# Performance work log

Measured on AMD Instinct MI355X. Metric: run time of the kernel, lower is better.

Reference implementation:

```python
import jax, jax.numpy as jnp
import numpy as np
from jax import lax

B, N, C = 8, 3136, 512
NUM_HEADS = 8
HEAD_DIM = C // NUM_HEADS
KS = 5  # depthwise conv kernel size


def setup_inputs() -> dict:
    key = jax.random.key(0)
    ks = jax.random.split(key, 8)
    s = 0.02
    return {
        "x": jax.random.normal(ks[0], (B, N, C), dtype=jnp.float32),
        "H": 56,
        "W": 56,
        "Wq": jax.random.normal(ks[1], (C, C), dtype=jnp.float32) * s,
        "Wkv": jax.random.normal(ks[2], (C, 2 * C), dtype=jnp.float32) * s,
        "pos_enc": jnp.zeros((1, N, C), dtype=jnp.float32),
        "dwc_w": jax.random.normal(ks[3], (HEAD_DIM, 1, KS, KS), dtype=jnp.float32) * s,
        "dwc_b": jnp.zeros((HEAD_DIM,), dtype=jnp.float32),
        "Wproj": jax.random.normal(ks[4], (C, C), dtype=jnp.float32) * s,
        "bproj": jnp.zeros((C,), dtype=jnp.float32),
    }


def _split_heads(t):
    # (B, N, C) -> (B*h, N, head_dim), matching 'b n (h c) -> (b h) n c'
    b, n, c = t.shape
    return t.reshape(b, n, NUM_HEADS, HEAD_DIM).transpose(0, 2, 1, 3).reshape(b * NUM_HEADS, n, HEAD_DIM)


def reference(x, H, W, Wq, Wkv, pos_enc, dwc_w, dwc_b, Wproj, bproj):
    b, n, c = x.shape
    # projections (qkv_bias=False)
    q = jnp.maximum(x @ Wq, 0.0)                       # ReLU kernel feature map
    kv = x @ Wkv
    k = jnp.maximum(kv[..., :c] + pos_enc, 0.0)
    v = kv[..., c:]

    q = _split_heads(q)  # (bh, n, d)
    k = _split_heads(k)
    v = _split_heads(v)

    # normalizer z_i = 1 / (q_i . sum_j k_j + eps)
    z = 1.0 / (jnp.einsum('bic,bc->bi', q, k.sum(axis=1)) + 1e-6)
    # kv-first ordering (i*j*(c+d) > c*d*(i+j) for these shapes)
    kvmat = jnp.einsum('bjc,bjd->bcd', k, v)           # (bh, d, d)
    out = jnp.einsum('bic,bcd->bid', q, kvmat) * z[..., None]

    # depthwise conv residual on v: 'b (w h) c -> b c w h'
    num = int(round(n ** 0.5))
    fmap = v.reshape(-1, num, num, HEAD_DIM).transpose(0, 3, 1, 2)  # (bh, d, num, num)
    fmap = lax.conv_general_dilated(
        fmap, dwc_w, window_strides=(1, 1), padding='SAME',
        feature_group_count=HEAD_DIM,
        dimension_numbers=('NCHW', 'OIHW', 'NCHW'))
    fmap = fmap + dwc_b[None, :, None, None]
    fmap = fmap.transpose(0, 2, 3, 1).reshape(-1, n, HEAD_DIM)
    out = out + fmap

    # merge heads: '(b h) n c -> b n (h c)'
    out = out.reshape(b, NUM_HEADS, n, HEAD_DIM).transpose(0, 2, 1, 3).reshape(b, n, c)
    return out @ Wproj + bproj
```

## Files before the change

### kernel.cpp

```cpp
#include <hip/hip_runtime.h>
#include <stdint.h>

#define B_    8
#define N_    3136
#define C_    512
#define MTOT  25088

typedef __attribute__((ext_vector_type(8))) short bf16x8;
typedef __attribute__((ext_vector_type(4))) float f32x4;

__device__ __forceinline__ float bf2f(short s){
  union { float f; uint32_t u; } cv; cv.u = ((uint32_t)(uint16_t)s) << 16; return cv.f;
}
__device__ __forceinline__ short f2bf(float f){
  union { float f; uint32_t u; } cv; cv.f = f;
  uint32_t r = cv.u + 0x7FFFu + ((cv.u >> 16) & 1u);
  return (short)(r >> 16);
}

typedef const __attribute__((address_space(1))) void* gas1_t;
typedef __attribute__((address_space(3))) void* las3_t;
__device__ __forceinline__ void gld16(const void* g, void* l){
  __builtin_amdgcn_global_load_lds((gas1_t)g, (las3_t)l, 16, 0, 0);
}

#define BARR  __builtin_amdgcn_s_barrier()
#define SCHB  __builtin_amdgcn_sched_barrier(0)
#define VMC0  asm volatile("s_waitcnt vmcnt(0)" ::: "memory")
#define VMC4  asm volatile("s_waitcnt vmcnt(4)" ::: "memory")
#define VMC6  asm volatile("s_waitcnt vmcnt(6)" ::: "memory")
#define LGKM0  asm volatile("s_waitcnt lgkmcnt(0)" ::: "memory")
#define LGKM2  asm volatile("s_waitcnt lgkmcnt(2)" ::: "memory")
#define LGKM10 asm volatile("s_waitcnt lgkmcnt(10)" ::: "memory")

__global__ __launch_bounds__(256) void cvt_x(const float* __restrict__ x,
                                             short* __restrict__ xb, int n8){
  int i = blockIdx.x * 256 + threadIdx.x;
  if (i >= n8) return;
  const float4* p = (const float4*)x;
  float4 a = p[i*2], b = p[i*2+1];
  short o[8] = { f2bf(a.x), f2bf(a.y), f2bf(a.z), f2bf(a.w),
                 f2bf(b.x), f2bf(b.y), f2bf(b.z), f2bf(b.w) };
  *(bf16x8*)(xb + i*8) = *(bf16x8*)o;
}

__global__ __launch_bounds__(256) void tconv(const float* __restrict__ src,
                                             short* __restrict__ dst, int J){
  __shared__ float tile[32][33];
  int jb = blockIdx.x * 32, kb = blockIdx.y * 32;
  int tx = threadIdx.x & 31, ty = threadIdx.x >> 5;
#pragma unroll
  for (int r = 0; r < 32; r += 8)
    tile[ty + r][tx] = src[(size_t)(kb + ty + r) * J + jb + tx];
  __syncthreads();
#pragma unroll
  for (int r = 0; r < 32; r += 8)
    dst[(size_t)(jb + ty + r) * 512 + kb + tx] = f2bf(tile[tx][ty + r]);
}

__global__ __launch_bounds__(256) void conv_wT(const float* __restrict__ w,
                                               float* __restrict__ wt){
  int i = blockIdx.x * 256 + threadIdx.x;
  if (i < 1600) { int c = i / 25, tap = i - c * 25; wt[tap * 64 + c] = w[i]; }
}

template<int MODE, int NCT>
__global__ __launch_bounds__(512, 2)
void gemm_bf16(const short* __restrict__ A, const short* __restrict__ Bt,
               short* __restrict__ oQ, short* __restrict__ oK, short* __restrict__ oV,
               const float* __restrict__ posenc,
               float* __restrict__ oF, const float* __restrict__ bias)
{
  extern __shared__ __align__(16) char lds[];
  const int tid = threadIdx.x;
  const int wave = tid >> 6, lane = tid & 63;
  const int fr = lane & 15;

  constexpr int nwg = 98 * NCT;
  constexpr int q8 = nwg / 8, r8 = nwg % 8;
  const int orig = blockIdx.x;
  const int xcd = orig & 7, lid = orig >> 3;
  const int swz = (xcd < r8 ? xcd * (q8 + 1) : r8 * (q8 + 1) + (xcd - r8) * q8) + lid;
  const int rt = (swz / NCT) * 256;
  const int ct = (swz % NCT) * 256;

  const int wm = (wave >> 2) * 128;
  const int wn = (wave & 3) * 64;

  const int srow = lane >> 2;
  const int csrc = ((lane & 3) ^ ((lane >> 3) & 3)) << 3;
  const short* srcA = A  + (size_t)(rt + wave * 32 + srow) * 512 + csrc;
  const short* srcB = Bt + (size_t)(ct + wave * 32 + srow) * 512 + csrc;
  char* dA = lds + wave * 2048;
  char* dB = lds + 32768 + wave * 2048;

  auto stage = [&](int sbb, int isB, int ks, int tt) {
    const short* s = (isB ? srcB : srcA) + tt * 64 + ks * 32;
    char* d = (isB ? dB : dA) + sbb + ks * 16384;
    gld16(s,        d);
    gld16(s + 8192, d + 1024);
  };

  const int cR   = (((lane >> 4) ^ ((fr >> 1) & 3)) << 4);
  const int offA = (wm + fr) * 64 + cR;
  const int offB = 32768 + (wn + fr) * 64 + cR;

#define READ_A(dst, bufb, ks) do { \
    const char* _p = lds + (bufb) + (ks) * 16384 + offA; \
    _Pragma("unroll") \
    for (int _i = 0; _i < 8; _i++) dst[_i] = *(const bf16x8*)(_p + _i * 1024); \
  } while (0)
#define READ_B2(dst, bufb, ks, j0) do { \
    const char* _p = lds + (bufb) + (ks) * 16384 + offB + (j0) * 1024; \
    dst[0] = *(const bf16x8*)(_p); \
    dst[1] = *(const bf16x8*)(_p + 1024); \
  } while (0)
#define MFMA16(afv, bv, jb) do { \
    __builtin_amdgcn_s_setprio(1); \
    _Pragma("unroll") \
    for (int _i = 0; _i < 8; _i++) { \
      acc[_i][jb]     = __builtin_amdgcn_mfma_f32_16x16x32_bf16(afv[_i], bv[0], acc[_i][jb],     0, 0, 0); \
      acc[_i][jb + 1] = __builtin_amdgcn_mfma_f32_16x16x32_bf16(afv[_i], bv[1], acc[_i][jb + 1], 0, 0, 0); \
    } \
    __builtin_amdgcn_s_setprio(0); \
  } while (0)

  f32x4 zv = {0.f, 0.f, 0.f, 0.f};
  f32x4 acc[8][4];
#pragma unroll
  for (int i = 0; i < 8; i++)
#pragma unroll
    for (int j = 0; j < 4; j++) acc[i][j] = zv;

  bf16x8 afU[8], afV[8], bX[2], bY[2];

  stage(0, 0, 0, 0); stage(0, 1, 0, 0); stage(0, 0, 1, 0); stage(0, 1, 1, 0);
  VMC4; BARR; SCHB;
  READ_A(afU, 0, 0);
  READ_B2(bX, 0, 0, 0);

  for (int t = 0; t < 7; ++t) {
    const int bufb = (t & 1) * 65536, sbb = bufb ^ 65536;
    stage(sbb, 0, 0, t + 1);
    VMC6; BARR; SCHB;
    READ_B2(bY, bufb, 0, 2);
    LGKM2; SCHB;
    MFMA16(afU, bX, 0);
    stage(sbb, 1, 0, t + 1);
    VMC4; BARR; SCHB;
    READ_A(afV, bufb, 1);
    READ_B2(bX, bufb, 1, 0);
    LGKM10; SCHB;
    MFMA16(afU, bY, 2);
    stage(sbb, 0, 1, t + 1);
    VMC6; BARR; SCHB;
    READ_B2(bY, bufb, 1, 2);
    LGKM2; SCHB;
    MFMA16(afV, bX, 0);
    stage(sbb, 1, 1, t + 1);
    VMC4; BARR; SCHB;
    READ_A(afU, sbb, 0);
    READ_B2(bX, sbb, 0, 0);
    LGKM10; SCHB;
    MFMA16(afV, bY, 2);
  }
  {
    const int bufb = 65536;
    VMC4; BARR; SCHB;
    READ_B2(bY, bufb, 0, 2);
    LGKM2; SCHB;
    MFMA16(afU, bX, 0);
    VMC0; BARR; SCHB;
    READ_A(afV, bufb, 1);
    READ_B2(bX, bufb, 1, 0);
    LGKM10; SCHB;
    MFMA16(afU, bY, 2);
    READ_B2(bY, bufb, 1, 2);
    LGKM2; SCHB;
    MFMA16(afV, bX, 0);
    LGKM0; SCHB;
    MFMA16(afV, bY, 2);
  }

  BARR; SCHB;

  const int rb = (lane >> 4) << 2;
  if (MODE == 0) {
    short* ov = (short*)lds;
    const int sel = ct >> 9;
    const int cb  = ct - sel * 512;
    short* outp = sel == 0 ? oQ : (sel == 1 ? oK : oV);
#pragma unroll
    for (int q4 = 0; q4 < 4; ++q4) {
      if (q4) __syncthreads();
      if ((wave >> 2) == (q4 >> 1)) {
        const int ib = (q4 & 1) * 4;
#pragma unroll
        for (int ii = 0; ii < 4; ii++)
#pragma unroll
          for (int j = 0; j < 4; j++)
#pragma unroll
            for (int r = 0; r < 4; r++)
              ov[(ii * 16 + rb + r) * 260 + wn + j * 16 + fr] = f2bf(acc[ib + ii][j][r]);
      }
      __syncthreads();
#pragma unroll
      for (int p = 0; p < 4; ++p) {
        int id = tid + 512 * p;
        int row = id >> 5, cc = (id & 31) * 8;
        bf16x8 vv = *(const bf16x8*)&ov[row * 260 + cc];
        int grow = rt + q4 * 64 + row;
        short o[8];
        if (sel == 0) {
#pragma unroll
          for (int e = 0; e < 8; e++) o[e] = f2bf(fmaxf(bf2f(vv[e]), 0.f));
        } else if (sel == 1) {
          int nr = grow % N_;
          const float* pp = posenc + (size_t)nr * 512 + cb + cc;
          f32x4 p0 = *(const f32x4*)pp;
          f32x4 p1 = *(const f32x4*)(pp + 4);
#pragma unroll
          for (int e = 0; e < 4; e++) {
            o[e]     = f2bf(fmaxf(bf2f(vv[e]) + p0[e], 0.f));
            o[e + 4] = f2bf(fmaxf(bf2f(vv[e + 4]) + p1[e], 0.f));
          }
        } else {
#pragma unroll
          for (int e = 0; e < 8; e++) o[e] = vv[e];
        }
        *(bf16x8*)(outp + (size_t)grow * 512 + cb + cc) = *(bf16x8*)o;
      }
    }
  } else {
    float* ovf = (float*)lds;
#pragma unroll
    for (int q4 = 0; q4 < 4; ++q4) {
      if (q4) __syncthreads();
      if ((wave >> 2) == (q4 >> 1)) {
        const int ib = (q4 & 1) * 4;
#pragma unroll
        for (int ii = 0; ii < 4; ii++)
#pragma unroll
          for (int j = 0; j < 4; j++)
#pragma unroll
            for (int r = 0; r < 4; r++)
              ovf[(ii * 16 + rb + r) * 260 + wn + j * 16 + fr] = acc[ib + ii][j][r];
      }
      __syncthreads();
#pragma unroll
      for (int p = 0; p < 4; ++p) {
        int id = tid + 512 * p;
        int row = id >> 5, cc = (id & 31) * 8;
        f32x4 v0 = *(const f32x4*)&ovf[row * 260 + cc];
        f32x4 v1 = *(const f32x4*)&ovf[row * 260 + cc + 4];
        v0 += *(const f32x4*)&bias[ct + cc];
        v1 += *(const f32x4*)&bias[ct + cc + 4];
        float* op = oF + (size_t)(rt + q4 * 64 + row) * 512 + ct + cc;
        *(f32x4*)op       = v0;
        *(f32x4*)(op + 4) = v1;
      }
    }
  }
#undef READ_A
#undef READ_B2
#undef MFMA16
}

__global__ __launch_bounds__(256)
void kvmat_part(const short* __restrict__ kb, const short* __restrict__ vb,
                float* __restrict__ pKV, float* __restrict__ pKS)
{
  __shared__ __align__(16) float lk[64][64];
  __shared__ __align__(16) float lv[64][64];
  const int chunk = blockIdx.x, bh = blockIdx.y;
  const int b = bh >> 3, h = bh & 7;
  const int t = threadIdx.x;
  const int tc = t >> 4, td = t & 15;
  const int kc = t & 63, kr = (t >> 6) * 16;
  float acc[4][4] = {};
  float ksacc = 0.f;

  for (int tile = 0; tile < 7; ++tile) {
    const int r0 = chunk * 448 + tile * 64;
    __syncthreads();
#pragma unroll
    for (int i = 0; i < 2; i++) {
      int idx = t + i * 256;
      int r = idx >> 3, c8 = (idx & 7) << 3;
      size_t g = (size_t)(b * N_ + r0 + r) * 512 + h * 64 + c8;
      bf16x8 kk = *(const bf16x8*)(kb + g);
      bf16x8 vv = *(const bf16x8*)(vb + g);
#pragma unroll
      for (int e = 0; e < 8; e++) { lk[r][c8 + e] = bf2f(kk[e]); lv[r][c8 + e] = bf2f(vv[e]); }
    }
    __syncthreads();
#pragma unroll 4
    for (int r = 0; r < 64; r++) {
      f32x4 k4 = *(const f32x4*)&lk[r][tc * 4];
      f32x4 v4 = *(const f32x4*)&lv[r][td * 4];
#pragma unroll
      for (int i = 0; i < 4; i++)
#pragma unroll
        for (int j = 0; j < 4; j++) acc[i][j] += k4[i] * v4[j];
    }
#pragma unroll 4
    for (int rr = 0; rr < 16; rr++) ksacc += lk[kr + rr][kc];
  }

  const int pbase = (bh * 7 + chunk) * 4096;
#pragma unroll
  for (int i = 0; i < 4; i++)
#pragma unroll
    for (int j = 0; j < 4; j++)
      pKV[pbase + (tc * 4 + i) * 64 + td * 4 + j] = acc[i][j];
  __syncthreads();
  float* red = &lk[0][0];
  red[t] = ksacc;
  __syncthreads();
  if (t < 64)
    pKS[(bh * 7 + chunk) * 64 + t] = red[t] + red[t + 64] + red[t + 128] + red[t + 192];
}

__global__ __launch_bounds__(256)
void kv_reduce(const float* __restrict__ pKV, const float* __restrict__ pKS,
               float* __restrict__ kvm, float* __restrict__ ksum)
{
  int bh = blockIdx.x, t = threadIdx.x;
#pragma unroll
  for (int i = 0; i < 16; i++) {
    int idx = t + i * 256;
    float s = 0.f;
#pragma unroll
    for (int c = 0; c < 7; c++) s += pKV[(bh * 7 + c) * 4096 + idx];
    kvm[bh * 4096 + idx] = s;
  }
  if (t < 64) {
    float s = 0.f;
#pragma unroll
    for (int c = 0; c < 7; c++) s += pKS[(bh * 7 + c) * 64 + t];
    ksum[bh * 64 + t] = s;
  }
}

__global__ __launch_bounds__(256)
void conv_dw(const short* __restrict__ vb, const float* __restrict__ wT,
             const float* __restrict__ bias, short* __restrict__ pre)
{
  __shared__ __align__(16) short lsv[5 * 56 * 64];
  __shared__ __align__(16) float lwT[25 * 64];
  const int y = blockIdx.x, bh = blockIdx.y;
  const int b = bh >> 3, h = bh & 7;
  const int t = threadIdx.x;
  for (int i = t; i < 1600; i += 256) lwT[i] = wT[i];
  for (int i = t; i < 2240; i += 256) {
    int row = i / 448, rem = i - row * 448;
    int xx = rem >> 3, c8i = rem & 7;
    int gy = y + row - 2;
    bf16x8 val = {0, 0, 0, 0, 0, 0, 0, 0};
    if ((unsigned)gy < 56u)
      val = *(const bf16x8*)(vb + (size_t)(b * N_ + gy * 56 + xx) * 512 + h * 64 + c8i * 8);
    *(bf16x8*)(lsv + i * 8) = val;
  }
  __syncthreads();

  const int c8 = t & 7;
  const int x0 = t >> 3;
  float acc0[8], acc1[8];
  {
    f32x4 b0 = *(const f32x4*)&bias[c8 * 8];
    f32x4 b1 = *(const f32x4*)&bias[c8 * 8 + 4];
#pragma unroll
    for (int e = 0; e < 4; e++) { acc0[e] = b0[e]; acc0[e+4] = b1[e];
                                  acc1[e] = b0[e]; acc1[e+4] = b1[e]; }
  }
#pragma unroll
  for (int dy = 0; dy < 5; ++dy) {
#pragma unroll
    for (int dx = 0; dx < 5; ++dx) {
      float w8[8];
      {
        const float* wp = &lwT[(dy * 5 + dx) * 64 + c8 * 8];
        *(f32x4*)&w8[0] = *(const f32x4*)wp;
        *(f32x4*)&w8[4] = *(const f32x4*)(wp + 4);
      }
      const int base = dy * 56 * 64 + c8 * 8;
      int xxa = x0 + dx - 2;
      if ((unsigned)xxa < 56u) {
        bf16x8 v = *(const bf16x8*)(lsv + base + xxa * 64);
#pragma unroll
        for (int e = 0; e < 8; e++) acc0[e] += bf2f(v[e]) * w8[e];
      }
      int xxb = xxa + 32;
      if (xxb < 56) {
        bf16x8 v = *(const bf16x8*)(lsv + base + xxb * 64);
#pragma unroll
        for (int e = 0; e < 8; e++) acc1[e] += bf2f(v[e]) * w8[e];
      }
    }
  }
  size_t gbase = (size_t)(b * N_ + y * 56 + x0) * 512 + h * 64 + c8 * 8;
  short o[8];
#pragma unroll
  for (int e = 0; e < 8; e++) o[e] = f2bf(acc0[e]);
  *(bf16x8*)(pre + gbase) = *(bf16x8*)o;
  if (x0 + 32 < 56) {
#pragma unroll
    for (int e = 0; e < 8; e++) o[e] = f2bf(acc1[e]);
    *(bf16x8*)(pre + gbase + (size_t)32 * 512) = *(bf16x8*)o;
  }
}

__global__ __launch_bounds__(256)
void attn_comb(const short* __restrict__ qb, const float* __restrict__ kvm,
               const float* __restrict__ ksum, short* __restrict__ pre)
{
  __shared__ __align__(16) float lkv[4096];
  __shared__ __align__(16) float lq[4096];
  __shared__ float lks[64];
  const int pt = blockIdx.x, bh = blockIdx.y;
  const int b = bh >> 3, h = bh & 7;
  const int t = threadIdx.x;
  for (int i = t; i < 4096; i += 256) lkv[i] = kvm[bh * 4096 + i];
  if (t < 64) lks[t] = ksum[bh * 64 + t];
  {
    const int p = t & 63, cg = t >> 6;
    size_t g = (size_t)(b * N_ + pt * 64 + p) * 512 + h * 64 + cg * 16;
    bf16x8 qa = *(const bf16x8*)(qb + g);
    bf16x8 qc = *(const bf16x8*)(qb + g + 8);
#pragma unroll
    for (int e = 0; e < 8; e++) {
      lq[(cg * 16 + e) * 64 + p]     = bf2f(qa[e]);
      lq[(cg * 16 + 8 + e) * 64 + p] = bf2f(qc[e]);
    }
  }
  __syncthreads();
  const int p = t & 63, d0 = (t >> 6) * 16;
  float acc[16] = {};
  float zd = 0.f;
#pragma unroll 4
  for (int c = 0; c < 64; c++) {
    float qv = lq[c * 64 + p];
    zd += qv * lks[c];
    const f32x4* row = (const f32x4*)&lkv[c * 64 + d0];
    f32x4 m0 = row[0], m1 = row[1], m2 = row[2], m3 = row[3];
#pragma unroll
    for (int e = 0; e < 4; e++) {
      acc[e]      += qv * m0[e];
      acc[4 + e]  += qv * m1[e];
      acc[8 + e]  += qv * m2[e];
      acc[12 + e] += qv * m3[e];
    }
  }
  float z = 1.f / (zd + 1e-6f);
  size_t base = (size_t)(b * N_ + pt * 64 + p) * 512 + h * 64 + d0;
  bf16x8 f0 = *(const bf16x8*)(pre + base);
  bf16x8 f1 = *(const bf16x8*)(pre + base + 8);
  short o[16];
#pragma unroll
  for (int e = 0; e < 8; e++) {
    o[e]     = f2bf(acc[e] * z + bf2f(f0[e]));
    o[e + 8] = f2bf(acc[e + 8] * z + bf2f(f1[e]));
  }
  *(bf16x8*)(pre + base)     = *(bf16x8*)&o[0];
  *(bf16x8*)(pre + base + 8) = *(bf16x8*)&o[8];
}

extern "C" void kernel_launch(void* const* d_in, const int* in_sizes, int n_in,
                              void* d_out, int out_size, void* d_ws, size_t ws_size,
                              hipStream_t stream)
{
  const float* x     = (const float*)d_in[0];
  const float* Wq    = (const float*)d_in[3];
  const float* Wkv   = (const float*)d_in[4];
  const float* pos   = (const float*)d_in[5];
  const float* dwcw  = (const float*)d_in[6];
  const float* dwcb  = (const float*)d_in[7];
  const float* Wproj = (const float*)d_in[8];
  const float* bproj = (const float*)d_in[9];
  float* out = (float*)d_out;

  char* ws = (char*)d_ws;
  size_t off = 0;
  auto alloc = [&](size_t bytes) -> void* {
    void* p = ws + off;
    off = (off + bytes + 255) & ~(size_t)255;
    return p;
  };
  short* xb     = (short*)alloc((size_t)MTOT * 512 * 2);
  short* wqkvT  = (short*)alloc((size_t)1536 * 512 * 2);
  short* wprojT = (short*)alloc((size_t)512 * 512 * 2);
  float* wTc    = (float*)alloc((size_t)25 * 64 * 4);
  short* qb     = (short*)alloc((size_t)MTOT * 512 * 2);
  short* kbuf   = (short*)alloc((size_t)MTOT * 512 * 2);
  short* vbuf   = (short*)alloc((size_t)MTOT * 512 * 2);
  float* pKV    = (float*)alloc((size_t)64 * 7 * 4096 * 4);
  float* pKS    = (float*)alloc((size_t)64 * 7 * 64 * 4);
  float* kvm    = (float*)alloc((size_t)64 * 4096 * 4);
  float* ksumB  = (float*)alloc((size_t)64 * 64 * 4);
  short* pre    = (short*)alloc((size_t)MTOT * 512 * 2);
  if (ws_size < off) return;

  {
    auto k0 = gemm_bf16<0, 6>;
    auto k1 = gemm_bf16<1, 2>;
    hipFuncSetAttribute(reinterpret_cast<const void*>(k0),
                        hipFuncAttributeMaxDynamicSharedMemorySize, 131072);
    hipFuncSetAttribute(reinterpret_cast<const void*>(k1),
                        hipFuncAttributeMaxDynamicSharedMemorySize, 131072);
  }

  cvt_x<<<dim3((MTOT * 512 / 8 + 255) / 256), dim3(256), 0, stream>>>(x, xb, MTOT * 512 / 8);
  conv_wT<<<dim3(7), dim3(256), 0, stream>>>(dwcw, wTc);
  tconv<<<dim3(16, 16), dim3(256), 0, stream>>>(Wq,    wqkvT,              512);
  tconv<<<dim3(32, 16), dim3(256), 0, stream>>>(Wkv,   wqkvT + 512 * 512, 1024);
  tconv<<<dim3(16, 16), dim3(256), 0, stream>>>(Wproj, wprojT,             512);
  gemm_bf16<0, 6><<<dim3(588), dim3(512), 131072, stream>>>(xb, wqkvT, qb, kbuf, vbuf, pos,
                                                            nullptr, nullptr);
  kvmat_part<<<dim3(7, 64), dim3(256), 0, stream>>>(kbuf, vbuf, pKV, pKS);
  kv_reduce<<<dim3(64), dim3(256), 0, stream>>>(pKV, pKS, kvm, ksumB);
  conv_dw<<<dim3(56, 64), dim3(256), 0, stream>>>(vbuf, wTc, dwcb, pre);
  attn_comb<<<dim3(49, 64), dim3(256), 0, stream>>>(qb, kvm, ksumB, pre);
  gemm_bf16<1, 2><<<dim3(196), dim3(512), 131072, stream>>>(pre, wprojT, nullptr, nullptr, nullptr,
                                                            nullptr, out, bproj);
}
```

Baseline: 234.1 us.

## Compute q·kvmat with bf16 MFMA using a transposed bf16 kv matrix

kv_reduce now writes the per-head kv matrix as a transposed bf16 array instead of fp32. The attention-combine kernel is replaced by a single-wavefront MFMA kernel that loads q and kvT fragments directly from global memory. It then stages the results through LDS for coalesced residual add and store. This removes the scalar FMA loop and the fp32 LDS staging of q and kv, at the cost of rounding kvmat to bf16 and using small 64-thread blocks.

```diff
diff --git a/kernel.cpp b/kernel.cpp
--- a/kernel.cpp
+++ b/kernel.cpp
@@ -323,7 +323,7 @@
 
 __global__ __launch_bounds__(256)
 void kv_reduce(const float* __restrict__ pKV, const float* __restrict__ pKS,
-               float* __restrict__ kvm, float* __restrict__ ksum)
+               short* __restrict__ kvT, float* __restrict__ ksum)
 {
   int bh = blockIdx.x, t = threadIdx.x;
 #pragma unroll
@@ -332,7 +332,8 @@
     float s = 0.f;
 #pragma unroll
     for (int c = 0; c < 7; c++) s += pKV[(bh * 7 + c) * 4096 + idx];
-    kvm[bh * 4096 + idx] = s;
+    int cc = idx >> 6, d = idx & 63;
+    kvT[bh * 4096 + d * 64 + cc] = f2bf(s);
   }
   if (t < 64) {
     float s = 0.f;
@@ -410,59 +411,80 @@
   }
 }
 
-__global__ __launch_bounds__(256)
-void attn_comb(const short* __restrict__ qb, const float* __restrict__ kvm,
+__global__ __launch_bounds__(64)
+void attn_mfma(const short* __restrict__ qb, const short* __restrict__ kvT,
                const float* __restrict__ ksum, short* __restrict__ pre)
 {
-  __shared__ __align__(16) float lkv[4096];
-  __shared__ __align__(16) float lq[4096];
+  __shared__ __align__(16) float ov[64 * 68];
   __shared__ float lks[64];
   const int pt = blockIdx.x, bh = blockIdx.y;
   const int b = bh >> 3, h = bh & 7;
-  const int t = threadIdx.x;
-  for (int i = t; i < 4096; i += 256) lkv[i] = kvm[bh * 4096 + i];
-  if (t < 64) lks[t] = ksum[bh * 64 + t];
-  {
-    const int p = t & 63, cg = t >> 6;
-    size_t g = (size_t)(b * N_ + pt * 64 + p) * 512 + h * 64 + cg * 16;
-    bf16x8 qa = *(const bf16x8*)(qb + g);
-    bf16x8 qc = *(const bf16x8*)(qb + g + 8);
-#pragma unroll
-    for (int e = 0; e < 8; e++) {
-      lq[(cg * 16 + e) * 64 + p]     = bf2f(qa[e]);
-      lq[(cg * 16 + 8 + e) * 64 + p] = bf2f(qc[e]);
-    }
-  }
+  const int l = threadIdx.x;
+  const int fr = l & 15, kg = l >> 4;
+  const int n0 = pt * 64;
+
+  lks[l] = ksum[bh * 64 + l];
+
+  const short* qbase = qb + (size_t)(b * N_ + n0) * 512 + h * 64;
+  const short* kvb   = kvT + bh * 4096;
+  bf16x8 af[4][2], bm[4][2];
+#pragma unroll
+  for (int i = 0; i < 4; i++)
+#pragma unroll
+    for (int s = 0; s < 2; s++) {
+      af[i][s] = *(const bf16x8*)(qbase + (size_t)(fr + i * 16) * 512 + s * 32 + kg * 8);
+      bm[i][s] = *(const bf16x8*)(kvb + (fr + i * 16) * 64 + s * 32 + kg * 8);
+    }
+
+  f32x4 zv4 = {0.f, 0.f, 0.f, 0.f};
+  f32x4 acc[4][4];
+#pragma unroll
+  for (int i = 0; i < 4; i++)
+#pragma unroll
+    for (int j = 0; j < 4; j++) acc[i][j] = zv4;
+#pragma unroll
+  for (int s = 0; s < 2; s++)
+#pragma unroll
+    for (int i = 0; i < 4; i++)
+#pragma unroll
+      for (int j = 0; j < 4; j++)
+        acc[i][j] = __builtin_amdgcn_mfma_f32_16x16x32_bf16(af[i][s], bm[j][s], acc[i][j], 0, 0, 0);
+
+  const short* qrow = qb + (size_t)(b * N_ + n0 + l) * 512 + h * 64;
+  float zd = 0.f;
+#pragma unroll
+  for (int g = 0; g < 8; g++) {
+    bf16x8 qv = *(const bf16x8*)(qrow + g * 8);
+#pragma unroll
+    for (int e = 0; e < 8; e++) zd += bf2f(qv[e]) * lks[g * 8 + e];
+  }
+  const float z = 1.f / (zd + 1e-6f);
+
+  const int rb = kg << 2;
+#pragma unroll
+  for (int i = 0; i < 4; i++)
+#pragma unroll
+    for (int j = 0; j < 4; j++)
+#pragma unroll
+      for (int r = 0; r < 4; r++)
+        ov[(i * 16 + rb + r) * 68 + j * 16 + fr] = acc[i][j][r];
   __syncthreads();
-  const int p = t & 63, d0 = (t >> 6) * 16;
-  float acc[16] = {};
-  float zd = 0.f;
-#pragma unroll 4
-  for (int c = 0; c < 64; c++) {
-    float qv = lq[c * 64 + p];
-    zd += qv * lks[c];
-    const f32x4* row = (const f32x4*)&lkv[c * 64 + d0];
-    f32x4 m0 = row[0], m1 = row[1], m2 = row[2], m3 = row[3];
+
+  size_t gb = (size_t)(b * N_ + n0 + l) * 512 + h * 64;
+  const float* ovr = &ov[l * 68];
+#pragma unroll
+  for (int g = 0; g < 8; g++) {
+    bf16x8 pv = *(const bf16x8*)(pre + gb + g * 8);
+    f32x4 a0 = *(const f32x4*)(ovr + g * 8);
+    f32x4 a1 = *(const f32x4*)(ovr + g * 8 + 4);
+    short o[8];
 #pragma unroll
     for (int e = 0; e < 4; e++) {
-      acc[e]      += qv * m0[e];
-      acc[4 + e]  += qv * m1[e];
-      acc[8 + e]  += qv * m2[e];
-      acc[12 + e] += qv * m3[e];
-    }
-  }
-  float z = 1.f / (zd + 1e-6f);
-  size_t base = (size_t)(b * N_ + pt * 64 + p) * 512 + h * 64 + d0;
-  bf16x8 f0 = *(const bf16x8*)(pre + base);
-  bf16x8 f1 = *(const bf16x8*)(pre + base + 8);
-  short o[16];
-#pragma unroll
-  for (int e = 0; e < 8; e++) {
-    o[e]     = f2bf(acc[e] * z + bf2f(f0[e]));
-    o[e + 8] = f2bf(acc[e + 8] * z + bf2f(f1[e]));
-  }
-  *(bf16x8*)(pre + base)     = *(bf16x8*)&o[0];
-  *(bf16x8*)(pre + base + 8) = *(bf16x8*)&o[8];
+      o[e]     = f2bf(a0[e] * z + bf2f(pv[e]));
+      o[e + 4] = f2bf(a1[e] * z + bf2f(pv[e + 4]));
+    }
+    *(bf16x8*)(pre + gb + g * 8) = *(bf16x8*)o;
+  }
 }
 
 extern "C" void kernel_launch(void* const* d_in, const int* in_sizes, int n_in,
@@ -495,7 +517,7 @@
   short* vbuf   = (short*)alloc((size_t)MTOT * 512 * 2);
   float* pKV    = (float*)alloc((size_t)64 * 7 * 4096 * 4);
   float* pKS    = (float*)alloc((size_t)64 * 7 * 64 * 4);
-  float* kvm    = (float*)alloc((size_t)64 * 4096 * 4);
+  short* kvT    = (short*)alloc((size_t)64 * 4096 * 2);
   float* ksumB  = (float*)alloc((size_t)64 * 64 * 4);
   short* pre    = (short*)alloc((size_t)MTOT * 512 * 2);
   if (ws_size < off) return;
@@ -517,9 +539,9 @@
   gemm_bf16<0, 6><<<dim3(588), dim3(512), 131072, stream>>>(xb, wqkvT, qb, kbuf, vbuf, pos,
                                                             nullptr, nullptr);
   kvmat_part<<<dim3(7, 64), dim3(256), 0, stream>>>(kbuf, vbuf, pKV, pKS);
-  kv_reduce<<<dim3(64), dim3(256), 0, stream>>>(pKV, pKS, kvm, ksumB);
+  kv_reduce<<<dim3(64), dim3(256), 0, stream>>>(pKV, pKS, kvT, ksumB);
   conv_dw<<<dim3(56, 64), dim3(256), 0, stream>>>(vbuf, wTc, dwcb, pre);
-  attn_comb<<<dim3(49, 64), dim3(256), 0, stream>>>(qb, kvm, ksumB, pre);
+  attn_mfma<<<dim3(49, 64), dim3(64), 0, stream>>>(qb, kvT, ksumB, pre);
   gemm_bf16<1, 2><<<dim3(196), dim3(512), 131072, stream>>>(pre, wprojT, nullptr, nullptr, nullptr,
                                                             nullptr, out, bproj);
 }
```

New measurement: 220.5 us. -5.8%, faster.
